# Performance work log

Hardware: AMD Instinct MI355X
Metric: run time of the kernel (lower is better)

The kernel has to match this reference:

```python
import jax, jax.numpy as jnp
import numpy as np

N = 50000      # nodes
E = 800000     # edges
D = 128        # input_dim
H = 128        # hidden_dim
OUT = 86       # output_dim (DDI classes)
P = 100000     # drug pairs
BN_EPS = 1e-5


def setup_inputs() -> dict:
    key = jax.random.key(0)
    ks = jax.random.split(key, 16)
    s = 0.05
    return {
        "x": jax.random.normal(ks[0], (N, D), jnp.float32),
        "edge_index": jax.random.randint(ks[1], (2, E), 0, N),
        "drug_pairs": jax.random.randint(ks[2], (P, 2), 0, N),
        # GCN layer 1 (input_dim -> hidden_dim) + BatchNorm params
        "W1": jax.random.normal(ks[3], (D, H), jnp.float32) * s,
        "b1": jnp.zeros((H,), jnp.float32),
        "gamma1": jnp.ones((H,), jnp.float32),
        "beta1": jnp.zeros((H,), jnp.float32),
        # GCN layer 2 (hidden -> hidden) + BatchNorm params
        "W2": jax.random.normal(ks[4], (H, H), jnp.float32) * s,
        "b2": jnp.zeros((H,), jnp.float32),
        "gamma2": jnp.ones((H,), jnp.float32),
        "beta2": jnp.zeros((H,), jnp.float32),
        # edge classifier MLP: Linear(2H,H) -> ReLU -> Linear(H,H//2) -> ReLU -> Linear(H//2,OUT)
        "Wc1": jax.random.normal(ks[5], (2 * H, H), jnp.float32) * s,
        "bc1": jnp.zeros((H,), jnp.float32),
        "Wc2": jax.random.normal(ks[6], (H, H // 2), jnp.float32) * s,
        "bc2": jnp.zeros((H // 2,), jnp.float32),
        "Wc3": jax.random.normal(ks[7], (H // 2, OUT), jnp.float32) * s,
        "bc3": jnp.zeros((OUT,), jnp.float32),
    }


def gcn_conv(h, W, b, src, dst, n):
    """PyG GCNConv: D^-1/2 (A + I) D^-1/2 (h @ W) + b, with self-loops added."""
    h = h @ W  # [N, H]
    ones = jnp.ones(src.shape[0], h.dtype)
    deg = jax.ops.segment_sum(ones, dst, num_segments=n) + 1.0  # in-degree + self loop
    dinv = jax.lax.rsqrt(deg)  # [N]
    coef = dinv[src] * dinv[dst]  # [E] edge normalization
    agg = jax.ops.segment_sum(h[src] * coef[:, None], dst, num_segments=n)
    agg = agg + h * (dinv * dinv)[:, None]  # self-loop contribution: deg_i^-1 * h_i
    return agg + b


def batch_norm(h, gamma, beta):
    # training-mode BatchNorm1d over node dim (biased variance)
    mean = jnp.mean(h, axis=0)
    var = jnp.mean((h - mean) ** 2, axis=0)
    return gamma * (h - mean) * jax.lax.rsqrt(var + BN_EPS) + beta


def reference(x, edge_index, drug_pairs, W1, b1, gamma1, beta1,
              W2, b2, gamma2, beta2, Wc1, bc1, Wc2, bc2, Wc3, bc3):
    src, dst = edge_index[0], edge_index[1]
    n = x.shape[0]
    # layer 1
    h = jax.nn.relu(batch_norm(gcn_conv(x, W1, b1, src, dst, n), gamma1, beta1))
    # layer 2
    h = jax.nn.relu(batch_norm(gcn_conv(h, W2, b2, src, dst, n), gamma2, beta2))
    # node-pair gather + concat -> edge classifier MLP (dropout = identity in eval)
    combined = jnp.concatenate([h[drug_pairs[:, 0]], h[drug_pairs[:, 1]]], axis=1)  # [P, 2H]
    z = jax.nn.relu(combined @ Wc1 + bc1)
    z = jax.nn.relu(z @ Wc2 + bc2)
    return z @ Wc3 + bc3  # [P, OUT]
```

## Files before the change

kernel.cpp:

```cpp
#include <hip/hip_runtime.h>
#include <cstdint>

#define N_NODES 50000
#define N_EDGES 800000
#define NPAIRS  100000

typedef unsigned short u16;
typedef unsigned int u32;
typedef unsigned long long u64;
typedef _Float16 f16;
typedef short short8v __attribute__((ext_vector_type(8)));
typedef _Float16 h8 __attribute__((ext_vector_type(8)));
typedef _Float16 h4 __attribute__((ext_vector_type(4)));
typedef float f32x4 __attribute__((ext_vector_type(4)));

static __device__ __forceinline__ u16 f2bf(float f) {
  unsigned int u = __float_as_uint(f);
  u += 0x7FFF + ((u >> 16) & 1);
  return (u16)(u >> 16);
}

static __device__ __forceinline__ float bits2f(u32 hi) {
  union { u16 b; f16 h; } x;
  x.b = (u16)hi;
  return (float)x.h;
}


__global__ __launch_bounds__(256) void wpack_k(const float* __restrict__ W1, const float* __restrict__ W2,
                                               const float* __restrict__ Wc1, const float* __restrict__ Wc2,
                                               const float* __restrict__ Wc3,
                                               f16* __restrict__ W1F, f16* __restrict__ W2F,
                                               u16* __restrict__ Wc1F, u16* __restrict__ Wc2F, u16* __restrict__ Wc3F) {
  int slot = blockIdx.x * 256 + threadIdx.x;
  int lane = slot & 63, j = lane & 15, kg = lane >> 4;
  if (slot < 2048) {
    int ks = (slot >> 6) & 3, nt = slot >> 8;
    int k0 = ks * 32 + kg * 8, c = nt * 16 + j;
#pragma unroll
    for (int e = 0; e < 8; e++) W1F[(size_t)slot * 8 + e] = (f16)W1[(k0 + e) * 128 + c];
  } else if (slot < 4096) {
    int s2 = slot - 2048;
    int ks = (s2 >> 6) & 3, nt = s2 >> 8;
    int k0 = ks * 32 + kg * 8, c = nt * 16 + j;
#pragma unroll
    for (int e = 0; e < 8; e++) W2F[(size_t)s2 * 8 + e] = (f16)W2[(k0 + e) * 128 + c];
  } else if (slot < 8192) {
    int s3 = slot - 4096;
    int ks = (s3 >> 6) & 7, nt = s3 >> 9;
    int k0 = ks * 32 + kg * 8, c = nt * 16 + j;
#pragma unroll
    for (int e = 0; e < 8; e++) Wc1F[(size_t)s3 * 8 + e] = f2bf(Wc1[(k0 + e) * 128 + c]);
  } else if (slot < 9216) {
    int s4 = slot - 8192;
    int ks = (s4 >> 6) & 3, nt = s4 >> 8;
    int k0 = ks * 32 + kg * 8, c = nt * 16 + j;
#pragma unroll
    for (int e = 0; e < 8; e++) Wc2F[(size_t)s4 * 8 + e] = f2bf(Wc2[(k0 + e) * 64 + c]);
  } else if (slot < 10240) {
    int s5 = slot - 9216;
    int ks = (s5 >> 6) & 1, nt = s5 >> 7;
    int k0 = ks * 32 + kg * 8, c = nt * 16 + j;
#pragma unroll
    for (int e = 0; e < 8; e++)
      Wc3F[(size_t)s5 * 8 + e] = f2bf((c < 86) ? Wc3[(k0 + e) * 86 + c] : 0.f);
  }
}


template<int MODE>
static __device__ __forceinline__ void gemm_body(const void* __restrict__ Ain,
                                                 const float* __restrict__ sums,
                                                 const float* __restrict__ gamma,
                                                 const float* __restrict__ beta,
                                                 const f16* __restrict__ WF,
                                                 f16* __restrict__ outh, int n, int row0,
                                                 f16* As, float* scsh) {
  int tid = threadIdx.x;
  if constexpr (MODE == 1) {
    if (tid < 128) {
      const float inv_n = 1.0f / (float)N_NODES;
      float mean = sums[tid] * inv_n;
      float var = sums[128 + tid] * inv_n - mean * mean;
      float sc = gamma[tid] * rsqrtf(var + 1e-5f);
      scsh[tid] = sc;
      scsh[128 + tid] = beta[tid] - mean * sc;
    }
    __syncthreads();
  }
#pragma unroll
  for (int it = 0; it < 8; it++) {
    int idx = it * 256 + tid;
    int r = idx >> 5, c4 = (idx & 31) * 4;
    int gr = row0 + r; if (gr >= n) gr = n - 1;
    float4 v;
    if constexpr (MODE == 0) {
      v = *(const float4*)&((const float*)Ain)[(size_t)gr * 128 + c4];
    } else {
      h4 hv4 = *(const h4*)&((const f16*)Ain)[(size_t)gr * 128 + c4];
      v.x = (float)hv4[0]; v.y = (float)hv4[1]; v.z = (float)hv4[2]; v.w = (float)hv4[3];
      v.x = fmaxf(v.x * scsh[c4 + 0] + scsh[128 + c4 + 0], 0.f);
      v.y = fmaxf(v.y * scsh[c4 + 1] + scsh[128 + c4 + 1], 0.f);
      v.z = fmaxf(v.z * scsh[c4 + 2] + scsh[128 + c4 + 2], 0.f);
      v.w = fmaxf(v.w * scsh[c4 + 3] + scsh[128 + c4 + 3], 0.f);
    }
    h4 hv; hv[0] = (f16)v.x; hv[1] = (f16)v.y; hv[2] = (f16)v.z; hv[3] = (f16)v.w;
    *(h4*)&As[r * 136 + c4] = hv;
  }
  __syncthreads();
  int w = tid >> 6, lane = tid & 63, li = lane & 15, kg = lane >> 4;
  f32x4 acc[4][2];
#pragma unroll
  for (int mt = 0; mt < 4; mt++)
#pragma unroll
    for (int ntl = 0; ntl < 2; ntl++)
#pragma unroll
      for (int q = 0; q < 4; q++) acc[mt][ntl][q] = 0.f;
#pragma unroll
  for (int ks = 0; ks < 4; ks++) {
    h8 a[4];
#pragma unroll
    for (int mt = 0; mt < 4; mt++)
      a[mt] = *(const h8*)&As[(mt * 16 + li) * 136 + kg * 8 + ks * 32];
#pragma unroll
    for (int ntl = 0; ntl < 2; ntl++) {
      int nt = 2 * w + ntl;
      h8 b = *(const h8*)&WF[((size_t)(nt * 4 + ks) * 64 + lane) * 8];
#pragma unroll
      for (int mt = 0; mt < 4; mt++)
        acc[mt][ntl] = __builtin_amdgcn_mfma_f32_16x16x32_f16(a[mt], b, acc[mt][ntl], 0, 0, 0);
    }
  }
  __syncthreads();
#pragma unroll
  for (int mt = 0; mt < 4; mt++)
#pragma unroll
    for (int ntl = 0; ntl < 2; ntl++)
#pragma unroll
      for (int r = 0; r < 4; r++)
        As[(mt * 16 + kg * 4 + r) * 136 + (2 * w + ntl) * 16 + li] = (f16)acc[mt][ntl][r];
  __syncthreads();
#pragma unroll
  for (int it = 0; it < 4; it++) {
    int idx = it * 256 + tid;
    int r = idx >> 4, c8 = (idx & 15) * 8;
    int gr = row0 + r;
    if (gr < n) *(h8*)&outh[(size_t)gr * 128 + c8] = *(const h8*)&As[r * 136 + c8];
  }
}


__global__ __launch_bounds__(256) void fused1_k(const int* __restrict__ ei, int* __restrict__ deg,
                                                int* __restrict__ rank,
                                                const float* __restrict__ x, const f16* __restrict__ W1F,
                                                f16* __restrict__ th, int n) {
  __shared__ f16 As[64 * 136];
  int b = blockIdx.x;
  if (b < N_EDGES / 256) {
    int e = b * 256 + threadIdx.x;
    rank[e] = atomicAdd(&deg[ei[N_EDGES + e]], 1);
    return;
  }
  gemm_body<0>(x, nullptr, nullptr, nullptr, W1F, th, n, (b - N_EDGES / 256) * 64, As, nullptr);
}


__global__ __launch_bounds__(256) void gemm2_k(const f16* __restrict__ Ain, const float* __restrict__ sums,
                                               const float* __restrict__ gamma, const float* __restrict__ beta,
                                               const f16* __restrict__ W2F, f16* __restrict__ th, int n) {
  __shared__ f16 As[64 * 136];
  __shared__ float scsh[256];
  gemm_body<1>(Ain, sums, gamma, beta, W2F, th, n, blockIdx.x * 64, As, scsh);
}

__global__ __launch_bounds__(1024) void scan_k(const int* __restrict__ deg, int* __restrict__ offs,
                                               float* __restrict__ dinv, int n) {
  __shared__ int wsum[16];
  __shared__ int wpre[16];
  __shared__ int run_s;
  int tid = threadIdx.x, lane = tid & 63, wid = tid >> 6;
  if (tid == 0) run_s = 0;
  __syncthreads();
  for (int base = 0; base < n; base += 8192) {
    int i8 = base + tid * 8;
    int v[8];
    if (i8 + 7 < n) {
      *(int4*)&v[0] = *(const int4*)&deg[i8];
      *(int4*)&v[4] = *(const int4*)&deg[i8 + 4];
    } else {
#pragma unroll
      for (int j = 0; j < 8; j++) v[j] = (i8 + j < n) ? deg[i8 + j] : 0;
    }
    int tsum = 0;
#pragma unroll
    for (int j = 0; j < 8; j++) tsum += v[j];
    int s = tsum;
#pragma unroll
    for (int d = 1; d < 64; d <<= 1) {
      int t = __shfl_up(s, d);
      if (lane >= d) s += t;
    }
    if (lane == 63) wsum[wid] = s;
    __syncthreads();
    if (tid == 0) {
      int acc = run_s;
#pragma unroll
      for (int w = 0; w < 16; w++) { wpre[w] = acc; acc += wsum[w]; }
      run_s = acc;
    }
    __syncthreads();
    int pre = wpre[wid] + (s - tsum);
    int o[8];
    o[0] = pre;
#pragma unroll
    for (int j = 1; j < 8; j++) o[j] = o[j - 1] + v[j - 1];
    float dv[8];
#pragma unroll
    for (int j = 0; j < 8; j++) dv[j] = rsqrtf((float)v[j] + 1.0f);
    if (i8 + 7 < n) {
      *(int4*)&offs[i8] = *(int4*)&o[0];
      *(int4*)&offs[i8 + 4] = *(int4*)&o[4];
      *(float4*)&dinv[i8] = *(float4*)&dv[0];
      *(float4*)&dinv[i8 + 4] = *(float4*)&dv[4];
    } else {
#pragma unroll
      for (int j = 0; j < 8; j++)
        if (i8 + j < n) { offs[i8 + j] = o[j]; dinv[i8 + j] = dv[j]; }
    }
    __syncthreads();
  }
  if (tid == 0) offs[n] = run_s;
}

__global__ __launch_bounds__(256) void fill_k(const int* __restrict__ ei, const int* __restrict__ offs,
                                              const int* __restrict__ rank, const float* __restrict__ dinv,
                                              u32* __restrict__ csrp, int E) {
  int e = blockIdx.x * 256 + threadIdx.x;
  if (e < E) {
    int s = ei[e], d = ei[E + e];
    int idx = offs[d] + rank[e];
    f16 hv = (f16)dinv[s];
    u32 pack = (u32)(u16)s | ((u32)(*(u16*)&hv) << 16);
    csrp[idx] = pack;
  }
}


__global__ __launch_bounds__(256) void agg_h_k(const f16* __restrict__ th, const float* __restrict__ dinv,
                                               const int* __restrict__ offs, const u32* __restrict__ csrp,
                                               const float* __restrict__ bias, f16* __restrict__ outh, int n) {
  int tid = threadIdx.x;
  int w = tid >> 6, lane = tid & 63;
  int half = lane >> 5, sl = lane & 31;
  int node = blockIdx.x * 4 + w;
  if (node >= n) return;
  const u64* hu8 = (const u64*)th;
  float di = dinv[node];
  int e0 = offs[node], e1 = offs[node + 1];
  union C8 { u64 u; f16 h[4]; };
  float a0[4] = {0.f, 0.f, 0.f, 0.f};
  float a1[4] = {0.f, 0.f, 0.f, 0.f};
  float a2[4] = {0.f, 0.f, 0.f, 0.f};
  float a3[4] = {0.f, 0.f, 0.f, 0.f};
  int e = e0;
  for (; e + 8 <= e1; e += 8) {
    u32 p0 = csrp[e + half];
    u32 p1 = csrp[e + 2 + half];
    u32 p2 = csrp[e + 4 + half];
    u32 p3 = csrp[e + 6 + half];
    C8 v0, v1, v2, v3;
    v0.u = hu8[(size_t)(p0 & 0xFFFF) * 32 + sl];
    v1.u = hu8[(size_t)(p1 & 0xFFFF) * 32 + sl];
    v2.u = hu8[(size_t)(p2 & 0xFFFF) * 32 + sl];
    v3.u = hu8[(size_t)(p3 & 0xFFFF) * 32 + sl];
    float c0 = bits2f(p0 >> 16), c1 = bits2f(p1 >> 16);
    float c2 = bits2f(p2 >> 16), c3 = bits2f(p3 >> 16);
#pragma unroll
    for (int j = 0; j < 4; j++) {
      a0[j] += c0 * (float)v0.h[j];
      a1[j] += c1 * (float)v1.h[j];
      a2[j] += c2 * (float)v2.h[j];
      a3[j] += c3 * (float)v3.h[j];
    }
  }
  for (; e < e1; e += 2) {
    int ee = e + half;
    bool valid = ee < e1;
    u32 p0 = csrp[valid ? ee : e];
    float c0 = valid ? bits2f(p0 >> 16) : 0.f;
    C8 v0; v0.u = hu8[(size_t)(p0 & 0xFFFF) * 32 + sl];
#pragma unroll
    for (int j = 0; j < 4; j++) a0[j] += c0 * (float)v0.h[j];
  }
  float s[4];
#pragma unroll
  for (int j = 0; j < 4; j++) {
    s[j] = (a0[j] + a1[j]) + (a2[j] + a3[j]);
    s[j] += __shfl_xor(s[j], 32);
  }
  if (half == 0) {
    C8 vs; vs.u = hu8[(size_t)node * 32 + sl];
    float4 b4 = *(const float4*)&bias[sl * 4];
    float sc = di * di;
    C8 o;
    o.h[0] = (f16)(di * s[0] + sc * (float)vs.h[0] + b4.x);
    o.h[1] = (f16)(di * s[1] + sc * (float)vs.h[1] + b4.y);
    o.h[2] = (f16)(di * s[2] + sc * (float)vs.h[2] + b4.z);
    o.h[3] = (f16)(di * s[3] + sc * (float)vs.h[3] + b4.w);
    ((u64*)outh)[(size_t)node * 32 + sl] = o.u;
  }
}


__global__ __launch_bounds__(256) void bn_stats_h_k(const f16* __restrict__ h, float* __restrict__ sums, int n) {
  int tid = threadIdx.x;
  int c = tid & 63, rg = tid >> 6;
  const u32* hu = (const u32*)h;
  union CV { u32 u; f16 h[2]; };
  float sx = 0.f, sy = 0.f, qx = 0.f, qy = 0.f;
  for (int r = blockIdx.x * 4 + rg; r < n; r += gridDim.x * 4) {
    CV v; v.u = hu[(size_t)r * 64 + c];
    float x = (float)v.h[0], y = (float)v.h[1];
    sx += x; qx += x * x;
    sy += y; qy += y * y;
  }
  __shared__ float rsum[4][128];
  __shared__ float rsq[4][128];
  rsum[rg][c * 2] = sx; rsum[rg][c * 2 + 1] = sy;
  rsq[rg][c * 2] = qx;  rsq[rg][c * 2 + 1] = qy;
  __syncthreads();
  if (tid < 128) {
    float a = (rsum[0][tid] + rsum[1][tid]) + (rsum[2][tid] + rsum[3][tid]);
    float b = (rsq[0][tid] + rsq[1][tid]) + (rsq[2][tid] + rsq[3][tid]);
    atomicAdd(&sums[tid], a);
    atomicAdd(&sums[128 + tid], b);
  }
}


#define SM_Z1 33792
#define SM_TOT (33792 + 17408)

__global__ __launch_bounds__(256) void classifier_k(const f16* __restrict__ hA, const float* __restrict__ sums,
    const float* __restrict__ gamma, const float* __restrict__ beta,
    const int* __restrict__ pairs,
    const u16* __restrict__ Wc1F, const float* __restrict__ bc1,
    const u16* __restrict__ Wc2F, const float* __restrict__ bc2,
    const u16* __restrict__ Wc3F, const float* __restrict__ bc3,
    float* __restrict__ out) {
  __shared__ __align__(16) char smem[SM_TOT];
  __shared__ int nodes[128];
  __shared__ float scsh[256];
  int tid = threadIdx.x;
  int p0 = blockIdx.x * 64;
  if (tid < 128) {
    int gi = p0 * 2 + tid;
    nodes[tid] = (gi < NPAIRS * 2) ? pairs[gi] : 0;
    const float inv_n = 1.0f / (float)N_NODES;
    float mean = sums[tid] * inv_n;
    float var = sums[128 + tid] * inv_n - mean * mean;
    float sc = gamma[tid] * rsqrtf(var + 1e-5f);
    scsh[tid] = sc;
    scsh[128 + tid] = beta[tid] - mean * sc;
  }
  __syncthreads();
  int w = tid >> 6, lane = tid & 63;
  int li = lane & 15, kg = lane >> 4;

  {
    unsigned int* cmb = (unsigned int*)smem;
    int c0 = lane * 2;
    float sc0 = scsh[c0], sh0 = scsh[128 + c0];
    float sc1 = scsh[c0 + 1], sh1 = scsh[128 + c0 + 1];
    union CV { u32 u; f16 h[2]; };
    for (int s = w * 32; s < w * 32 + 32; s++) {
      int nd = nodes[s];
      CV v; v.u = ((const u32*)hA)[(size_t)nd * 64 + lane];
      u32 b0 = f2bf(fmaxf((float)v.h[0] * sc0 + sh0, 0.f));
      u32 b1 = f2bf(fmaxf((float)v.h[1] * sc1 + sh1, 0.f));
      cmb[(s >> 1) * 132 + (s & 1) * 64 + lane] = b0 | (b1 << 16);
    }
  }
  __syncthreads();

  {
    f32x4 acc[4][2];
#pragma unroll
    for (int ntl = 0; ntl < 2; ntl++) {
      float b = bc1[(2 * w + ntl) * 16 + li];
#pragma unroll
      for (int mt = 0; mt < 4; mt++)
#pragma unroll
        for (int q = 0; q < 4; q++) acc[mt][ntl][q] = b;
    }
    for (int ks = 0; ks < 8; ks++) {
      short8v a[4];
#pragma unroll
      for (int mt = 0; mt < 4; mt++)
        a[mt] = *(const short8v*)(smem + (mt * 16 + li) * 528 + kg * 16 + ks * 64);
#pragma unroll
      for (int ntl = 0; ntl < 2; ntl++) {
        int nt = 2 * w + ntl;
        short8v b = *(const short8v*)(Wc1F + ((size_t)(nt * 8 + ks) * 64 + lane) * 8);
#pragma unroll
        for (int mt = 0; mt < 4; mt++)
          acc[mt][ntl] = __builtin_amdgcn_mfma_f32_16x16x32_bf16(a[mt], b, acc[mt][ntl], 0, 0, 0);
      }
    }
#pragma unroll
    for (int mt = 0; mt < 4; mt++)
#pragma unroll
      for (int ntl = 0; ntl < 2; ntl++)
#pragma unroll
        for (int r = 0; r < 4; r++) {
          int row = mt * 16 + kg * 4 + r;
          int col = (2 * w + ntl) * 16 + li;
          *(u16*)(smem + SM_Z1 + row * 272 + col * 2) = f2bf(fmaxf(acc[mt][ntl][r], 0.f));
        }
  }
  __syncthreads();

  {
    f32x4 acc[4];
    float b = bc2[w * 16 + li];
#pragma unroll
    for (int mt = 0; mt < 4; mt++)
#pragma unroll
      for (int q = 0; q < 4; q++) acc[mt][q] = b;
    for (int ks = 0; ks < 4; ks++) {
      short8v a[4];
#pragma unroll
      for (int mt = 0; mt < 4; mt++)
        a[mt] = *(const short8v*)(smem + SM_Z1 + (mt * 16 + li) * 272 + kg * 16 + ks * 64);
      short8v bf = *(const short8v*)(Wc2F + ((size_t)(w * 4 + ks) * 64 + lane) * 8);
#pragma unroll
      for (int mt = 0; mt < 4; mt++)
        acc[mt] = __builtin_amdgcn_mfma_f32_16x16x32_bf16(a[mt], bf, acc[mt], 0, 0, 0);
    }
#pragma unroll
    for (int mt = 0; mt < 4; mt++)
#pragma unroll
      for (int r = 0; r < 4; r++) {
        int row = mt * 16 + kg * 4 + r;
        int col = w * 16 + li;
        *(u16*)(smem + row * 144 + col * 2) = f2bf(fmaxf(acc[mt][r], 0.f));
      }
  }
  __syncthreads();

  {
    f32x4 acc[4][2];
#pragma unroll
    for (int ntl = 0; ntl < 2; ntl++) {
      int col = (2 * w + ntl) * 16 + li;
      float b = (col < 86) ? bc3[col] : 0.f;
#pragma unroll
      for (int mt = 0; mt < 4; mt++)
#pragma unroll
        for (int q = 0; q < 4; q++) acc[mt][ntl][q] = b;
    }
    for (int ks = 0; ks < 2; ks++) {
      short8v a[4];
#pragma unroll
      for (int mt = 0; mt < 4; mt++)
        a[mt] = *(const short8v*)(smem + (mt * 16 + li) * 144 + kg * 16 + ks * 64);
#pragma unroll
      for (int ntl = 0; ntl < 2; ntl++) {
        int nt = 2 * w + ntl;
        short8v bf = *(const short8v*)(Wc3F + ((size_t)(nt * 2 + ks) * 64 + lane) * 8);
#pragma unroll
        for (int mt = 0; mt < 4; mt++)
          acc[mt][ntl] = __builtin_amdgcn_mfma_f32_16x16x32_bf16(a[mt], bf, acc[mt][ntl], 0, 0, 0);
      }
    }
#pragma unroll
    for (int mt = 0; mt < 4; mt++)
#pragma unroll
      for (int ntl = 0; ntl < 2; ntl++) {
        int col = (2 * w + ntl) * 16 + li;
        if (col < 86) {
#pragma unroll
          for (int r = 0; r < 4; r++) {
            int row = p0 + mt * 16 + kg * 4 + r;
            if (row < NPAIRS) out[(size_t)row * 86 + col] = acc[mt][ntl][r];
          }
        }
      }
  }
}


extern "C" void kernel_launch(void* const* d_in, const int* in_sizes, int n_in,
                              void* d_out, int out_size, void* d_ws, size_t ws_size,
                              hipStream_t stream) {
  (void)in_sizes; (void)n_in; (void)out_size; (void)ws_size;
  const float* x   = (const float*)d_in[0];
  const int*   ei  = (const int*)d_in[1];
  const int* pairs = (const int*)d_in[2];
  const float* W1  = (const float*)d_in[3];
  const float* b1  = (const float*)d_in[4];
  const float* g1  = (const float*)d_in[5];
  const float* be1 = (const float*)d_in[6];
  const float* W2  = (const float*)d_in[7];
  const float* b2  = (const float*)d_in[8];
  const float* g2  = (const float*)d_in[9];
  const float* be2 = (const float*)d_in[10];
  const float* Wc1 = (const float*)d_in[11];
  const float* bc1 = (const float*)d_in[12];
  const float* Wc2 = (const float*)d_in[13];
  const float* bc2 = (const float*)d_in[14];
  const float* Wc3 = (const float*)d_in[15];
  const float* bc3 = (const float*)d_in[16];
  float* out = (float*)d_out;

  size_t off = 0;
  auto alloc = [&](size_t bytes) -> char* {
    char* p = (char*)d_ws + off;
    off += (bytes + 255) & ~(size_t)255;
    return p;
  };
  int* deg      = (int*)alloc(N_NODES * 4);
  float* sums1  = (float*)alloc(256 * 4);
  float* sums2  = (float*)alloc(256 * 4);
  size_t zero_span = off;
  int* offs     = (int*)alloc((N_NODES + 1) * 4);
  int* rank     = (int*)alloc(N_EDGES * 4);
  u32* csrp     = (u32*)alloc(N_EDGES * 4);
  float* dinv   = (float*)alloc(N_NODES * 4);
  f16* W1F      = (f16*)alloc(2048 * 8 * 2);
  f16* W2F      = (f16*)alloc(2048 * 8 * 2);
  u16* Wc1F     = (u16*)alloc(4096 * 8 * 2);
  u16* Wc2F     = (u16*)alloc(1024 * 8 * 2);
  u16* Wc3F     = (u16*)alloc(1024 * 8 * 2);
  f16* th       = (f16*)alloc((size_t)N_NODES * 128 * 2);
  f16* hA       = (f16*)alloc((size_t)N_NODES * 128 * 2);

  hipMemsetAsync(d_ws, 0, zero_span, stream);
  wpack_k<<<40, 256, 0, stream>>>(W1, W2, Wc1, Wc2, Wc3, W1F, W2F, Wc1F, Wc2F, Wc3F);

  fused1_k<<<N_EDGES / 256 + (N_NODES + 63) / 64, 256, 0, stream>>>(ei, deg, rank, x, W1F, th, N_NODES);
  scan_k<<<1, 1024, 0, stream>>>(deg, offs, dinv, N_NODES);
  fill_k<<<N_EDGES / 256, 256, 0, stream>>>(ei, offs, rank, dinv, csrp, N_EDGES);

  agg_h_k<<<(N_NODES + 3) / 4, 256, 0, stream>>>(th, dinv, offs, csrp, b1, hA, N_NODES);
  bn_stats_h_k<<<256, 256, 0, stream>>>(hA, sums1, N_NODES);

  gemm2_k<<<(N_NODES + 63) / 64, 256, 0, stream>>>(hA, sums1, g1, be1, W2F, th, N_NODES);
  agg_h_k<<<(N_NODES + 3) / 4, 256, 0, stream>>>(th, dinv, offs, csrp, b2, hA, N_NODES);
  bn_stats_h_k<<<256, 256, 0, stream>>>(hA, sums2, N_NODES);

  classifier_k<<<(NPAIRS + 63) / 64, 256, 0, stream>>>(hA, sums2, g2, be2, pairs,
                                                       Wc1F, bc1, Wc2F, bc2, Wc3F, bc3, out);
}
```

Measured before the change: 333.5 us.

## Precompute BN+ReLU bf16 node features and gather MFMA operands directly from global

Adds a separate kernel that applies the second BatchNorm, ReLU and the bf16 conversion once per node, writing into the reused th buffer. The classifier then loads its A operands straight from global memory per MFMA fragment instead of staging the gathered, normalized pair rows in shared memory, which removes one barrier and roughly a third of its LDS. This avoids normalizing each node again for every pair it appears in (200k gathers versus 50k nodes) and should allow more blocks per CU. The cost is an extra kernel launch plus a full 12.8 MB read and write pass, and A-operand loads become 16-byte scattered global reads.

New measurement: 338.5 us. Within noise of the previous version (+1.5%).

```diff
diff --git a/kernel.cpp b/kernel.cpp
--- a/kernel.cpp
+++ b/kernel.cpp
@@ -338,50 +338,57 @@
 }
 
 
-#define SM_Z1 33792
-#define SM_TOT (33792 + 17408)
-
-__global__ __launch_bounds__(256) void classifier_k(const f16* __restrict__ hA, const float* __restrict__ sums,
-    const float* __restrict__ gamma, const float* __restrict__ beta,
-    const int* __restrict__ pairs,
+__global__ __launch_bounds__(256) void bn_apply_bf16_k(const f16* __restrict__ h, const float* __restrict__ sums,
+                                                       const float* __restrict__ gamma, const float* __restrict__ beta,
+                                                       u16* __restrict__ hb) {
+  __shared__ float scsh[256];
+  int tid = threadIdx.x;
+  if (tid < 128) {
+    const float inv_n = 1.0f / (float)N_NODES;
+    float mean = sums[tid] * inv_n;
+    float var = sums[128 + tid] * inv_n - mean * mean;
+    float sc = gamma[tid] * rsqrtf(var + 1e-5f);
+    scsh[tid] = sc;
+    scsh[128 + tid] = beta[tid] - mean * sc;
+  }
+  __syncthreads();
+  int idx = blockIdx.x * 256 + tid;
+  int c0 = (idx & 31) * 4;
+  h4 v4 = *(const h4*)&h[(size_t)idx * 4];
+  ushort4 o;
+  o.x = f2bf(fmaxf((float)v4[0] * scsh[c0 + 0] + scsh[128 + c0 + 0], 0.f));
+  o.y = f2bf(fmaxf((float)v4[1] * scsh[c0 + 1] + scsh[128 + c0 + 1], 0.f));
+  o.z = f2bf(fmaxf((float)v4[2] * scsh[c0 + 2] + scsh[128 + c0 + 2], 0.f));
+  o.w = f2bf(fmaxf((float)v4[3] * scsh[c0 + 3] + scsh[128 + c0 + 3], 0.f));
+  *(ushort4*)&hb[(size_t)idx * 4] = o;
+}
+
+
+#define SM_Z2 17408
+#define SM_TOT (17408 + 9216)
+
+__global__ __launch_bounds__(256) void classifier_k(const u16* __restrict__ hbf, const int* __restrict__ pairs,
     const u16* __restrict__ Wc1F, const float* __restrict__ bc1,
     const u16* __restrict__ Wc2F, const float* __restrict__ bc2,
     const u16* __restrict__ Wc3F, const float* __restrict__ bc3,
     float* __restrict__ out) {
   __shared__ __align__(16) char smem[SM_TOT];
   __shared__ int nodes[128];
-  __shared__ float scsh[256];
   int tid = threadIdx.x;
   int p0 = blockIdx.x * 64;
   if (tid < 128) {
     int gi = p0 * 2 + tid;
     nodes[tid] = (gi < NPAIRS * 2) ? pairs[gi] : 0;
-    const float inv_n = 1.0f / (float)N_NODES;
-    float mean = sums[tid] * inv_n;
-    float var = sums[128 + tid] * inv_n - mean * mean;
-    float sc = gamma[tid] * rsqrtf(var + 1e-5f);
-    scsh[tid] = sc;
-    scsh[128 + tid] = beta[tid] - mean * sc;
   }
   __syncthreads();
   int w = tid >> 6, lane = tid & 63;
   int li = lane & 15, kg = lane >> 4;
-
-  {
-    unsigned int* cmb = (unsigned int*)smem;
-    int c0 = lane * 2;
-    float sc0 = scsh[c0], sh0 = scsh[128 + c0];
-    float sc1 = scsh[c0 + 1], sh1 = scsh[128 + c0 + 1];
-    union CV { u32 u; f16 h[2]; };
-    for (int s = w * 32; s < w * 32 + 32; s++) {
-      int nd = nodes[s];
-      CV v; v.u = ((const u32*)hA)[(size_t)nd * 64 + lane];
-      u32 b0 = f2bf(fmaxf((float)v.h[0] * sc0 + sh0, 0.f));
-      u32 b1 = f2bf(fmaxf((float)v.h[1] * sc1 + sh1, 0.f));
-      cmb[(s >> 1) * 132 + (s & 1) * 64 + lane] = b0 | (b1 << 16);
-    }
-  }
-  __syncthreads();
+  int na[4], nb[4];
+#pragma unroll
+  for (int mt = 0; mt < 4; mt++) {
+    na[mt] = nodes[2 * (mt * 16 + li)];
+    nb[mt] = nodes[2 * (mt * 16 + li) + 1];
+  }
 
   {
     f32x4 acc[4][2];
@@ -393,11 +400,14 @@
 #pragma unroll
         for (int q = 0; q < 4; q++) acc[mt][ntl][q] = b;
     }
+#pragma unroll
     for (int ks = 0; ks < 8; ks++) {
       short8v a[4];
 #pragma unroll
-      for (int mt = 0; mt < 4; mt++)
-        a[mt] = *(const short8v*)(smem + (mt * 16 + li) * 528 + kg * 16 + ks * 64);
+      for (int mt = 0; mt < 4; mt++) {
+        int nd = (ks < 4) ? na[mt] : nb[mt];
+        a[mt] = *(const short8v*)(hbf + (size_t)nd * 128 + (ks & 3) * 32 + kg * 8);
+      }
 #pragma unroll
       for (int ntl = 0; ntl < 2; ntl++) {
         int nt = 2 * w + ntl;
@@ -415,7 +425,7 @@
         for (int r = 0; r < 4; r++) {
           int row = mt * 16 + kg * 4 + r;
           int col = (2 * w + ntl) * 16 + li;
-          *(u16*)(smem + SM_Z1 + row * 272 + col * 2) = f2bf(fmaxf(acc[mt][ntl][r], 0.f));
+          *(u16*)(smem + row * 272 + col * 2) = f2bf(fmaxf(acc[mt][ntl][r], 0.f));
         }
   }
   __syncthreads();
@@ -431,7 +441,7 @@
       short8v a[4];
 #pragma unroll
       for (int mt = 0; mt < 4; mt++)
-        a[mt] = *(const short8v*)(smem + SM_Z1 + (mt * 16 + li) * 272 + kg * 16 + ks * 64);
+        a[mt] = *(const short8v*)(smem + (mt * 16 + li) * 272 + kg * 16 + ks * 64);
       short8v bf = *(const short8v*)(Wc2F + ((size_t)(w * 4 + ks) * 64 + lane) * 8);
 #pragma unroll
       for (int mt = 0; mt < 4; mt++)
@@ -443,7 +453,7 @@
       for (int r = 0; r < 4; r++) {
         int row = mt * 16 + kg * 4 + r;
         int col = w * 16 + li;
-        *(u16*)(smem + row * 144 + col * 2) = f2bf(fmaxf(acc[mt][r], 0.f));
+        *(u16*)(smem + SM_Z2 + row * 144 + col * 2) = f2bf(fmaxf(acc[mt][r], 0.f));
       }
   }
   __syncthreads();
@@ -463,7 +473,7 @@
       short8v a[4];
 #pragma unroll
       for (int mt = 0; mt < 4; mt++)
-        a[mt] = *(const short8v*)(smem + (mt * 16 + li) * 144 + kg * 16 + ks * 64);
+        a[mt] = *(const short8v*)(smem + SM_Z2 + (mt * 16 + li) * 144 + kg * 16 + ks * 64);
 #pragma unroll
       for (int ntl = 0; ntl < 2; ntl++) {
         int nt = 2 * w + ntl;
@@ -534,6 +544,7 @@
   u16* Wc3F     = (u16*)alloc(1024 * 8 * 2);
   f16* th       = (f16*)alloc((size_t)N_NODES * 128 * 2);
   f16* hA       = (f16*)alloc((size_t)N_NODES * 128 * 2);
+  u16* hbf      = (u16*)th;
 
   hipMemsetAsync(d_ws, 0, zero_span, stream);
   wpack_k<<<40, 256, 0, stream>>>(W1, W2, Wc1, Wc2, Wc3, W1F, W2F, Wc1F, Wc2F, Wc3F);
@@ -549,6 +560,7 @@
   agg_h_k<<<(N_NODES + 3) / 4, 256, 0, stream>>>(th, dinv, offs, csrp, b2, hA, N_NODES);
   bn_stats_h_k<<<256, 256, 0, stream>>>(hA, sums2, N_NODES);
 
-  classifier_k<<<(NPAIRS + 63) / 64, 256, 0, stream>>>(hA, sums2, g2, be2, pairs,
-                                                       Wc1F, bc1, Wc2F, bc2, Wc3F, bc3, out);
-}
+  bn_apply_bf16_k<<<(N_NODES * 128) / 1024, 256, 0, stream>>>(hA, sums2, g2, be2, hbf);
+
+  classifier_k<<<(NPAIRS + 63) / 64, 256, 0, stream>>>(hbf, pairs, Wc1F, bc1, Wc2F, bc2, Wc3F, bc3, out);
+}
```
